# Kernel optimization log

Hardware: AMD Instinct MI355X
Metric: run time of the kernel (lower is better)

Reference implementation:

```python
import jax, jax.numpy as jnp
import numpy as np

HIDDEN = 1024
HEADS = 16
HEAD_DIM = HIDDEN // HEADS


def setup_inputs() -> dict:
    key = jax.random.key(0)
    ks = jax.random.split(key, 9)
    B, S = 2, 2048
    std = 1.0 / np.sqrt(HIDDEN)
    inp = {
        'hidden_states': jax.random.normal(ks[0], (B, S, HIDDEN), dtype=jnp.float32),
        'attention_mask': jnp.ones((B, S), dtype=jnp.int32),
        'wq': jax.random.normal(ks[1], (HIDDEN, HIDDEN), dtype=jnp.float32) * std,
        'bq': jnp.zeros((HIDDEN,), dtype=jnp.float32),
        'wk': jax.random.normal(ks[2], (HIDDEN, HIDDEN), dtype=jnp.float32) * std,
        'bk': jnp.zeros((HIDDEN,), dtype=jnp.float32),
        'wv': jax.random.normal(ks[3], (HIDDEN, HIDDEN), dtype=jnp.float32) * std,
        'bv': jnp.zeros((HIDDEN,), dtype=jnp.float32),
        'wo': jax.random.normal(ks[4], (HIDDEN, HIDDEN), dtype=jnp.float32) * std,
        'bo': jnp.zeros((HIDDEN,), dtype=jnp.float32),
    }
    return inp


def reference(hidden_states, attention_mask, wq, bq, wk, bk, wv, bv, wo, bo):
    B, S, H = hidden_states.shape
    def heads(x):  # [B,S,H] -> [B,nh,S,hd]
        return x.reshape(B, S, HEADS, HEAD_DIM).transpose(0, 2, 1, 3)
    q = heads(hidden_states @ wq + bq)
    k = heads(hidden_states @ wk + bk)
    v = heads(hidden_states @ wv + bv)
    scores = jnp.einsum('bhqd,bhkd->bhqk', q, k) / np.sqrt(HEAD_DIM).astype(np.float32)
    causal = jnp.tril(jnp.ones((S, S), dtype=bool))  # True = keep
    keep = causal[None, None] & (attention_mask[:, None, None, :] != 0)
    scores = jnp.where(keep, scores, -jnp.inf)
    probs = jax.nn.softmax(scores, axis=-1)
    out = jnp.einsum('bhqk,bhkd->bhqd', probs, v)  # [B,nh,S,hd]
    out = out.transpose(0, 2, 1, 3).reshape(B, S, H)
    return out @ wo + bo
```

## Files before the change

kernel.cpp:

```cpp
#include <hip/hip_runtime.h>

#define HID   1024
#define SLEN  2048
#define NHEAD 16
#define HDIM  64
#define SC2L  0.18033688f

typedef unsigned short u16;
typedef _Float16 f16;
using bf16x8 = __attribute__((ext_vector_type(8))) short;
using f16x4  = __attribute__((ext_vector_type(4))) f16;
using f32x4  = __attribute__((ext_vector_type(4))) float;

typedef __attribute__((address_space(1))) void gvoid;
typedef __attribute__((address_space(3))) void lvoid;

__device__ __forceinline__ u16 f2bf(float f) {
  union { float f; unsigned u; } v; v.f = f;
  unsigned u = v.u;
  return (u16)((u + 0x7fffu + ((u >> 16) & 1u)) >> 16);
}

__device__ __forceinline__ void async_ld16(const u16* g, u16* l) {
  __builtin_amdgcn_global_load_lds((gvoid*)g, (lvoid*)l, 16, 0, 0);
}

__global__ __launch_bounds__(256) void prep_kernel(const float* __restrict__ x,
                                                   const float* __restrict__ wq,
                                                   const float* __restrict__ wk,
                                                   const float* __restrict__ wv,
                                                   const float* __restrict__ wo,
                                                   u16* __restrict__ xb,
                                                   u16* __restrict__ wt) {
  const int tid = threadIdx.x;
  if (blockIdx.z == 4) {
    const int bid = blockIdx.y * 32 + blockIdx.x;
#pragma unroll
    for (int it = 0; it < 4; ++it) {
      const int i = bid * 1024 + it * 256 + tid;
      float4 v = ((const float4*)x)[i];
      ushort4 o;
      o.x = f2bf(v.x); o.y = f2bf(v.y); o.z = f2bf(v.z); o.w = f2bf(v.w);
      ((ushort4*)xb)[i] = o;
    }
    return;
  }
  const float* src = (blockIdx.z == 0) ? wq : (blockIdx.z == 1) ? wk
                   : (blockIdx.z == 2) ? wv : wo;
  u16* dst = wt + (size_t)blockIdx.z * (HID * HID);
  __shared__ float tile[32][33];
  const int n0 = blockIdx.x * 32, k0 = blockIdx.y * 32;
  const int xx = tid & 31, yy = tid >> 5;
  for (int i = yy; i < 32; i += 8)
    tile[i][xx] = src[(size_t)(k0 + i) * HID + n0 + xx];
  __syncthreads();
  for (int i = yy; i < 32; i += 8)
    dst[(size_t)(n0 + i) * HID + k0 + xx] = f2bf(tile[xx][i]);
}

__global__ __launch_bounds__(256) void gemm_qkv_kernel(const u16* __restrict__ A,
                                                       const u16* __restrict__ Bt,
                                                       const float* __restrict__ bq,
                                                       const float* __restrict__ bk,
                                                       const float* __restrict__ bv,
                                                       u16* __restrict__ Qb,
                                                       u16* __restrict__ Kb,
                                                       u16* __restrict__ VTf) {
  __shared__ u16 smem[16384];
  const int tid  = threadIdx.x;
  const int wave = tid >> 6, lane = tid & 63;
  const int quad = lane >> 4, l16 = lane & 15;
  const int raw = blockIdx.y * 24 + blockIdx.x;
  const int logi = (raw & 7) * 96 + (raw >> 3);
  const int bx = logi % 24, by = logi / 24;
  const int n0g = bx * 128;
  const int region = bx >> 3;
  const int colbase = (bx & 7) * 128;
  const int m0 = by * 128;
  const int wm = (wave & 1) * 64, wn = (wave >> 1) * 64;

  f32x4 acc[4][4] = {};
  const int srow = lane >> 2;
  const int scol = (lane & 3) * 8;

#define STAGE_G(kt, bi)                                                          \
  for (int c = wave; c < 8; c += 4) {                                            \
    async_ld16(A  + (size_t)(m0  + c * 16 + srow) * HID + (kt) + scol,           \
               &smem[(bi) * 8192 + c * 512]);                                    \
    async_ld16(Bt + (size_t)(n0g + c * 16 + srow) * HID + (kt) + scol,           \
               &smem[(bi) * 8192 + 4096 + c * 512]);                             \
  }

  STAGE_G(0, 0);
  for (int ks = 0; ks < 32; ++ks) {
    const int bi = ks & 1;
    if (ks < 31) {
      STAGE_G((ks + 1) * 32, bi ^ 1);
      asm volatile("s_waitcnt vmcnt(4)" ::: "memory");
    } else {
      asm volatile("s_waitcnt vmcnt(0)" ::: "memory");
    }
    __builtin_amdgcn_s_barrier();

    const u16* sA = smem + bi * 8192;
    const u16* sB = smem + bi * 8192 + 4096;
    bf16x8 af[4], bfr[4];
#pragma unroll
    for (int t = 0; t < 4; ++t) {
      af[t]  = *(const bf16x8*)&sA[(wm + t * 16 + l16) * 32 + quad * 8];
      bfr[t] = *(const bf16x8*)&sB[(wn + t * 16 + l16) * 32 + quad * 8];
    }
#pragma unroll
    for (int mt = 0; mt < 4; ++mt)
#pragma unroll
      for (int nt = 0; nt < 4; ++nt)
        acc[mt][nt] = __builtin_amdgcn_mfma_f32_16x16x32_bf16(af[mt], bfr[nt],
                                                              acc[mt][nt], 0, 0, 0);
    __builtin_amdgcn_s_barrier();
  }
#undef STAGE_G

  const float* bias = (region == 0) ? bq : (region == 1) ? bk : bv;
  float bvv[4];
#pragma unroll
  for (int nt = 0; nt < 4; ++nt) bvv[nt] = bias[colbase + wn + nt * 16 + l16];

  if (region == 2) {
    const int bb = m0 >> 11;
    const int m0loc = m0 & 2047;
    const int h0 = colbase >> 6;
    u16* T = smem;
#pragma unroll
    for (int h2 = 0; h2 < 2; ++h2) {
      __syncthreads();
      if ((wave >> 1) == h2) {
#pragma unroll
        for (int mt = 0; mt < 4; ++mt)
#pragma unroll
          for (int nt = 0; nt < 4; ++nt)
#pragma unroll
            for (int r = 0; r < 4; ++r) {
              const int sl = (wave & 1) * 64 + mt * 16 + quad * 4 + r;
              const int dl = nt * 16 + l16;
              union { f16 h; u16 u; } cv;
              cv.h = (f16)(acc[mt][nt][r] + bvv[nt]);
              T[dl * 128 + (((sl >> 3) ^ l16) * 8) + (sl & 7)] = cv.u;
            }
      }
      __syncthreads();
      const int d = tid >> 2, sg = (tid & 3) * 4;
      u16* slab0 = VTf + ((size_t)((bb * NHEAD + h0 + h2) * 128 + (m0loc >> 4))) * 1024;
#pragma unroll
      for (int cc = 0; cc < 4; ++cc) {
        const int cl = sg + cc;
        const int ph = cl ^ (d & 15);
        const int slot = (d * 2 + (cl & 1)) ^ ((d >> 2) & 1);
        *(bf16x8*)(slab0 + (size_t)(cl >> 1) * 1024 + slot * 8)
            = *(const bf16x8*)&T[d * 128 + ph * 8];
      }
    }
    return;
  }

  u16* C = (region == 0) ? Qb : Kb;
#pragma unroll
  for (int mt = 0; mt < 4; ++mt)
#pragma unroll
    for (int r = 0; r < 4; ++r) {
      const int row = m0 + wm + mt * 16 + quad * 4 + r;
#pragma unroll
      for (int nt = 0; nt < 4; ++nt) {
        const int col = colbase + wn + nt * 16 + l16;
        C[(size_t)row * HID + col] = f2bf(acc[mt][nt][r] + bvv[nt]);
      }
    }
}

__global__ __launch_bounds__(256) void gemm_o_kernel(const u16* __restrict__ A,
                                                     const u16* __restrict__ Bt,
                                                     const float* __restrict__ bias,
                                                     float* __restrict__ Cf) {
  __shared__ u16 smem[12288];
  const int tid  = threadIdx.x;
  const int wave = tid >> 6, lane = tid & 63;
  const int quad = lane >> 4, l16 = lane & 15;
  const int raw = blockIdx.y * 8 + blockIdx.x;
  const int logi = (raw & 7) * 64 + (raw >> 3);
  const int n0 = (logi & 7) * 128;
  const int m0 = (logi >> 3) * 64;
  const int wn = wave * 32;

  f32x4 acc[4][2] = {};
  const int srow = lane >> 2;
  const int scol = (lane & 3) * 8;

#define STAGE_O(kt, bi)                                                          \
  for (int c = wave; c < 12; c += 4) {                                           \
    if (c < 4) async_ld16(A + (size_t)(m0 + c * 16 + srow) * HID + (kt) + scol,  \
                          &smem[(bi) * 6144 + c * 512]);                         \
    else async_ld16(Bt + (size_t)(n0 + (c - 4) * 16 + srow) * HID + (kt) + scol, \
                    &smem[(bi) * 6144 + 2048 + (c - 4) * 512]);                  \
  }

  STAGE_O(0, 0);
  for (int ks = 0; ks < 32; ++ks) {
    const int bi = ks & 1;
    if (ks < 31) {
      STAGE_O((ks + 1) * 32, bi ^ 1);
      asm volatile("s_waitcnt vmcnt(3)" ::: "memory");
    } else {
      asm volatile("s_waitcnt vmcnt(0)" ::: "memory");
    }
    __builtin_amdgcn_s_barrier();

    const u16* sA = smem + bi * 6144;
    const u16* sB = smem + bi * 6144 + 2048;
    bf16x8 af[4], bfr[2];
#pragma unroll
    for (int t = 0; t < 4; ++t)
      af[t] = *(const bf16x8*)&sA[(t * 16 + l16) * 32 + quad * 8];
#pragma unroll
    for (int t = 0; t < 2; ++t)
      bfr[t] = *(const bf16x8*)&sB[(wn + t * 16 + l16) * 32 + quad * 8];
#pragma unroll
    for (int mt = 0; mt < 4; ++mt)
#pragma unroll
      for (int nt = 0; nt < 2; ++nt)
        acc[mt][nt] = __builtin_amdgcn_mfma_f32_16x16x32_bf16(af[mt], bfr[nt],
                                                              acc[mt][nt], 0, 0, 0);
    __builtin_amdgcn_s_barrier();
  }
#undef STAGE_O

  float bvv[2];
#pragma unroll
  for (int nt = 0; nt < 2; ++nt) bvv[nt] = bias[n0 + wn + nt * 16 + l16];
#pragma unroll
  for (int mt = 0; mt < 4; ++mt)
#pragma unroll
    for (int r = 0; r < 4; ++r) {
      const int row = m0 + mt * 16 + quad * 4 + r;
#pragma unroll
      for (int nt = 0; nt < 2; ++nt)
        Cf[(size_t)row * HID + n0 + wn + nt * 16 + l16] = acc[mt][nt][r] + bvv[nt];
    }
}

__global__ __launch_bounds__(256, 2) void flash_attn_kernel(const u16* __restrict__ Q,
                                                            const u16* __restrict__ K,
                                                            const u16* __restrict__ VT,
                                                            const int* __restrict__ mask,
                                                            u16* __restrict__ O) {
  const int xb = blockIdx.x, h = blockIdx.y, b = blockIdx.z;
  const int tid  = threadIdx.x;
  const int wave = tid >> 6, lane = tid & 63;
  const int quad = lane >> 4, l16 = lane & 15;

  __shared__ alignas(16) char smraw[35840];
  u16*   Ks  = (u16*)smraw;
  u16*   Vt  = (u16*)(smraw + 16384);
  float* Ob0 = (float*)smraw;
  float* Ob1 = (float*)(smraw + 16896);
  float* lb  = (float*)(smraw + 33792);

  const u16* Kh  = K  + (size_t)b * SLEN * HID + h * HDIM;
  const u16* Vth = VT + (size_t)(b * NHEAD + h) * (128 * 1024);

  const int srow8 = lane >> 3;
  const int gch   = (lane & 7) ^ srow8;
  const int rx    = l16 & 7;

  for (int phase = 0; phase < 2; ++phase) {
    const int qt = phase ? (31 - xb) : xb;
    const int q0 = qt * 64;

    bf16x8 qb[4][2];
#pragma unroll
    for (int nt = 0; nt < 4; ++nt) {
      const u16* qp = Q + (size_t)(b * SLEN + q0 + nt * 16 + l16) * HID + h * HDIM + quad * 8;
      qb[nt][0] = *(const bf16x8*)qp;
      qb[nt][1] = *(const bf16x8*)(qp + 32);
    }

    f32x4 oacc[4][4] = {};
    float l_part[4] = {0.f, 0.f, 0.f, 0.f};

    {
      const int r0 = wave * 16 + srow8;
      u16* kd = Ks + wave * 1024;
      async_ld16(Kh + (size_t)r0 * HID + gch * 8,       kd);
      async_ld16(Kh + (size_t)(r0 + 8) * HID + gch * 8, kd + 512);
      const u16* vs = Vth + (size_t)wave * 1024;
      u16* vd = Vt + wave * 1024;
      async_ld16(vs + lane * 8,        vd);
      async_ld16(vs + (64 + lane) * 8, vd + 512);
    }
    int4 mi = *(const int4*)(mask + b * SLEN + wave * 16 + quad * 4);

    for (int j = 0; j <= qt; ++j) {
      const int buf = j & 1;
      u16* KsB = Ks + buf * 4096;
      u16* VtB = Vt + buf * 4096;

      int4 mi_n = mi;
      if (j < qt) {
        const int nb = (buf ^ 1) * 4096;
        const int jn = j + 1;
        const int r0 = wave * 16 + srow8;
        u16* kd = Ks + nb + wave * 1024;
        async_ld16(Kh + (size_t)(jn * 64 + r0) * HID + gch * 8,     kd);
        async_ld16(Kh + (size_t)(jn * 64 + r0 + 8) * HID + gch * 8, kd + 512);
        const u16* vs = Vth + (size_t)(jn * 4 + wave) * 1024;
        u16* vd = Vt + nb + wave * 1024;
        async_ld16(vs + lane * 8,        vd);
        async_ld16(vs + (64 + lane) * 8, vd + 512);
        asm volatile("s_waitcnt vmcnt(4)" ::: "memory");
        mi_n = *(const int4*)(mask + b * SLEN + jn * 64 + wave * 16 + quad * 4);
      } else {
        asm volatile("s_waitcnt vmcnt(0)" ::: "memory");
      }

      float map[4];
      map[0] = mi.x ? 0.f : -1e30f;  map[1] = mi.y ? 0.f : -1e30f;
      map[2] = mi.z ? 0.f : -1e30f;  map[3] = mi.w ? 0.f : -1e30f;

      const u16* kp = KsB + (wave * 16 + l16) * 64;
      const int ph0 = quad ^ rx;
      const bf16x8 ka0 = *(const bf16x8*)(kp + ph0 * 8);
      const bf16x8 ka1 = *(const bf16x8*)(kp + (ph0 ^ 4) * 8);

      float p[4][4];
#pragma unroll
      for (int nt = 0; nt < 4; ++nt) {
        f32x4 z = {0.f, 0.f, 0.f, 0.f};
        z = __builtin_amdgcn_mfma_f32_16x16x32_bf16(ka0, qb[nt][0], z, 0, 0, 0);
        z = __builtin_amdgcn_mfma_f32_16x16x32_bf16(ka1, qb[nt][1], z, 0, 0, 0);
#pragma unroll
        for (int r = 0; r < 4; ++r)
          p[nt][r] = exp2f(fmaf(z[r], SC2L, map[r]));
      }
      if (j == qt) {
#pragma unroll
        for (int nt = 0; nt < 4; ++nt)
#pragma unroll
          for (int r = 0; r < 4; ++r)
            if (wave * 16 + quad * 4 + r > nt * 16 + l16) p[nt][r] = 0.f;
      }

      f16x4 pb[4];
#pragma unroll
      for (int nt = 0; nt < 4; ++nt) {
        l_part[nt] += (p[nt][0] + p[nt][1]) + (p[nt][2] + p[nt][3]);
        pb[nt][0] = (f16)p[nt][0]; pb[nt][1] = (f16)p[nt][1];
        pb[nt][2] = (f16)p[nt][2]; pb[nt][3] = (f16)p[nt][3];
      }

#pragma unroll
      for (int dt = 0; dt < 4; ++dt) {
        const int dd = dt * 16 + l16;
        const int slot = (dd * 2 + (quad >> 1)) ^ ((dd >> 2) & 1);
        const f16x4 va = *(const f16x4*)(VtB + wave * 1024 + slot * 8 + (quad & 1) * 4);
#pragma unroll
        for (int nt = 0; nt < 4; ++nt)
          oacc[dt][nt] = __builtin_amdgcn_mfma_f32_16x16x16f16(va, pb[nt], oacc[dt][nt], 0, 0, 0);
      }
      mi = mi_n;
    }

    __syncthreads();

#pragma unroll
    for (int nt = 0; nt < 4; ++nt) {
      l_part[nt] += __shfl_xor(l_part[nt], 16);
      l_part[nt] += __shfl_xor(l_part[nt], 32);
    }
    if (quad == 0)
#pragma unroll
      for (int nt = 0; nt < 4; ++nt) lb[wave * 64 + nt * 16 + l16] = l_part[nt];

    if ((wave & 1) == 0) {
      float* ob = (wave == 0) ? Ob0 : Ob1;
#pragma unroll
      for (int dt = 0; dt < 4; ++dt)
#pragma unroll
        for (int nt = 0; nt < 4; ++nt)
#pragma unroll
          for (int r = 0; r < 4; ++r)
            ob[(dt * 16 + quad * 4 + r) * 66 + nt * 16 + l16] = oacc[dt][nt][r];
    }
    __syncthreads();
    if (wave & 1) {
      float* ob = (wave == 1) ? Ob0 : Ob1;
#pragma unroll
      for (int dt = 0; dt < 4; ++dt)
#pragma unroll
        for (int nt = 0; nt < 4; ++nt)
#pragma unroll
          for (int r = 0; r < 4; ++r)
            ob[(dt * 16 + quad * 4 + r) * 66 + nt * 16 + l16] += oacc[dt][nt][r];
    }
    __syncthreads();

    {
      const int q  = tid >> 2;
      const int dc = tid & 3;
      const float l = lb[q] + lb[64 + q] + lb[128 + q] + lb[192 + q];
      const float inv = 1.f / l;
      u16 ob[16];
#pragma unroll
      for (int e = 0; e < 16; ++e) {
        const int d = dc * 16 + e;
        ob[e] = f2bf((Ob0[d * 66 + q] + Ob1[d * 66 + q]) * inv);
      }
      u16* op = O + (size_t)(b * SLEN + q0 + q) * HID + h * HDIM + dc * 16;
      *(bf16x8*)op       = *(bf16x8*)&ob[0];
      *(bf16x8*)(op + 8) = *(bf16x8*)&ob[8];
    }
    __syncthreads();
  }
}

extern "C" void kernel_launch(void* const* d_in, const int* in_sizes, int n_in,
                              void* d_out, int out_size, void* d_ws, size_t ws_size,
                              hipStream_t stream) {
  const float* x    = (const float*)d_in[0];
  const int*   mask = (const int*)d_in[1];
  const float* wq   = (const float*)d_in[2];
  const float* bq   = (const float*)d_in[3];
  const float* wk   = (const float*)d_in[4];
  const float* bk   = (const float*)d_in[5];
  const float* wv   = (const float*)d_in[6];
  const float* bv   = (const float*)d_in[7];
  const float* wo   = (const float*)d_in[8];
  const float* bo   = (const float*)d_in[9];
  float* out = (float*)d_out;

  char* ws = (char*)d_ws;
  u16* XBF = (u16*)(ws);
  u16* WT  = (u16*)(ws + (8u  << 20));
  u16* QBF = (u16*)(ws + (16u << 20));
  u16* KBF = (u16*)(ws + (24u << 20));
  u16* VTF = (u16*)(ws + (32u << 20));
  u16* ATT = (u16*)(ws);

  prep_kernel<<<dim3(32, 32, 5), 256, 0, stream>>>(x, wq, wk, wv, wo, XBF, WT);
  gemm_qkv_kernel<<<dim3(24, 32), 256, 0, stream>>>(XBF, WT, bq, bk, bv, QBF, KBF, VTF);
  flash_attn_kernel<<<dim3(16, NHEAD, 2), 256, 0, stream>>>(QBF, KBF, VTF, mask, ATT);
  gemm_o_kernel<<<dim3(8, 64), 256, 0, stream>>>(ATT, WT + (3u << 20), bo, out);
}
```

Before: 196.7 us.

## Use 8 waves and a 4-stage async load pipeline in QKV GEMM

The QKV projection GEMM now launches 512 threads per block. Each of the 8 waves computes a 64x32 sub-tile instead of a 64x64 one, and half the waves load A while the other half load B. The shared-memory ring goes from double to quad buffering, prefetching three k-steps ahead with adjusted vmcnt waits, to hide global load latency and raise wave occupancy. The cost is twice the LDS (64 KB per block), which may limit how many blocks fit per CU, and each wave issues fewer MFMAs per LDS fragment it reads.

```diff
diff --git a/kernel.cpp b/kernel.cpp
--- a/kernel.cpp
+++ b/kernel.cpp
@@ -58,7 +58,7 @@
     dst[(size_t)(n0 + i) * HID + k0 + xx] = f2bf(tile[xx][i]);
 }
 
-__global__ __launch_bounds__(256) void gemm_qkv_kernel(const u16* __restrict__ A,
+__global__ __launch_bounds__(512) void gemm_qkv_kernel(const u16* __restrict__ A,
                                                        const u16* __restrict__ Bt,
                                                        const float* __restrict__ bq,
                                                        const float* __restrict__ bk,
@@ -66,7 +66,7 @@
                                                        u16* __restrict__ Qb,
                                                        u16* __restrict__ Kb,
                                                        u16* __restrict__ VTf) {
-  __shared__ u16 smem[16384];
+  __shared__ u16 smem[32768];
   const int tid  = threadIdx.x;
   const int wave = tid >> 6, lane = tid & 63;
   const int quad = lane >> 4, l16 = lane & 15;
@@ -77,26 +77,42 @@
   const int region = bx >> 3;
   const int colbase = (bx & 7) * 128;
   const int m0 = by * 128;
-  const int wm = (wave & 1) * 64, wn = (wave >> 1) * 64;
-
-  f32x4 acc[4][4] = {};
+  const int wm = (wave & 1) * 64;
+  const int wn = (wave >> 1) * 32;
+
+  f32x4 acc[4][2] = {};
   const int srow = lane >> 2;
   const int scol = (lane & 3) * 8;
 
 #define STAGE_G(kt, bi)                                                          \
-  for (int c = wave; c < 8; c += 4) {                                            \
-    async_ld16(A  + (size_t)(m0  + c * 16 + srow) * HID + (kt) + scol,           \
-               &smem[(bi) * 8192 + c * 512]);                                    \
-    async_ld16(Bt + (size_t)(n0g + c * 16 + srow) * HID + (kt) + scol,           \
-               &smem[(bi) * 8192 + 4096 + c * 512]);                             \
+  {                                                                              \
+    u16* dstb = smem + (bi) * 8192;                                              \
+    const int c0 = 2 * wave, c1 = 2 * wave + 1;                                  \
+    if (wave < 4) {                                                              \
+      async_ld16(A + (size_t)(m0 + c0 * 16 + srow) * HID + (kt) + scol,          \
+                 &dstb[c0 * 512]);                                               \
+      async_ld16(A + (size_t)(m0 + c1 * 16 + srow) * HID + (kt) + scol,          \
+                 &dstb[c1 * 512]);                                               \
+    } else {                                                                     \
+      async_ld16(Bt + (size_t)(n0g + (c0 - 8) * 16 + srow) * HID + (kt) + scol,  \
+                 &dstb[4096 + (c0 - 8) * 512]);                                  \
+      async_ld16(Bt + (size_t)(n0g + (c1 - 8) * 16 + srow) * HID + (kt) + scol,  \
+                 &dstb[4096 + (c1 - 8) * 512]);                                  \
+    }                                                                            \
   }
 
   STAGE_G(0, 0);
+  STAGE_G(32, 1);
+  STAGE_G(64, 2);
   for (int ks = 0; ks < 32; ++ks) {
-    const int bi = ks & 1;
-    if (ks < 31) {
-      STAGE_G((ks + 1) * 32, bi ^ 1);
+    const int bi = ks & 3;
+    if (ks <= 28) {
+      STAGE_G((ks + 3) * 32, (ks + 3) & 3);
+      asm volatile("s_waitcnt vmcnt(6)" ::: "memory");
+    } else if (ks == 29) {
       asm volatile("s_waitcnt vmcnt(4)" ::: "memory");
+    } else if (ks == 30) {
+      asm volatile("s_waitcnt vmcnt(2)" ::: "memory");
     } else {
       asm volatile("s_waitcnt vmcnt(0)" ::: "memory");
     }
@@ -104,16 +120,17 @@
 
     const u16* sA = smem + bi * 8192;
     const u16* sB = smem + bi * 8192 + 4096;
-    bf16x8 af[4], bfr[4];
-#pragma unroll
-    for (int t = 0; t < 4; ++t) {
+    bf16x8 af[4], bfr[2];
+#pragma unroll
+    for (int t = 0; t < 4; ++t)
       af[t]  = *(const bf16x8*)&sA[(wm + t * 16 + l16) * 32 + quad * 8];
+#pragma unroll
+    for (int t = 0; t < 2; ++t)
       bfr[t] = *(const bf16x8*)&sB[(wn + t * 16 + l16) * 32 + quad * 8];
-    }
 #pragma unroll
     for (int mt = 0; mt < 4; ++mt)
 #pragma unroll
-      for (int nt = 0; nt < 4; ++nt)
+      for (int nt = 0; nt < 2; ++nt)
         acc[mt][nt] = __builtin_amdgcn_mfma_f32_16x16x32_bf16(af[mt], bfr[nt],
                                                               acc[mt][nt], 0, 0, 0);
     __builtin_amdgcn_s_barrier();
@@ -121,9 +138,9 @@
 #undef STAGE_G
 
   const float* bias = (region == 0) ? bq : (region == 1) ? bk : bv;
-  float bvv[4];
-#pragma unroll
-  for (int nt = 0; nt < 4; ++nt) bvv[nt] = bias[colbase + wn + nt * 16 + l16];
+  float bvv[2];
+#pragma unroll
+  for (int nt = 0; nt < 2; ++nt) bvv[nt] = bias[colbase + wn + nt * 16 + l16];
 
   if (region == 2) {
     const int bb = m0 >> 11;
@@ -133,25 +150,25 @@
 #pragma unroll
     for (int h2 = 0; h2 < 2; ++h2) {
       __syncthreads();
-      if ((wave >> 1) == h2) {
+      if ((wave >> 2) == h2) {
 #pragma unroll
         for (int mt = 0; mt < 4; ++mt)
 #pragma unroll
-          for (int nt = 0; nt < 4; ++nt)
+          for (int nt = 0; nt < 2; ++nt)
 #pragma unroll
             for (int r = 0; r < 4; ++r) {
-              const int sl = (wave & 1) * 64 + mt * 16 + quad * 4 + r;
-              const int dl = nt * 16 + l16;
+              const int sl = wm + mt * 16 + quad * 4 + r;
+              const int dl = (wn & 32) + nt * 16 + l16;
               union { f16 h; u16 u; } cv;
               cv.h = (f16)(acc[mt][nt][r] + bvv[nt]);
               T[dl * 128 + (((sl >> 3) ^ l16) * 8) + (sl & 7)] = cv.u;
             }
       }
       __syncthreads();
-      const int d = tid >> 2, sg = (tid & 3) * 4;
+      const int d = tid >> 3, sg = (tid & 7) * 2;
       u16* slab0 = VTf + ((size_t)((bb * NHEAD + h0 + h2) * 128 + (m0loc >> 4))) * 1024;
 #pragma unroll
-      for (int cc = 0; cc < 4; ++cc) {
+      for (int cc = 0; cc < 2; ++cc) {
         const int cl = sg + cc;
         const int ph = cl ^ (d & 15);
         const int slot = (d * 2 + (cl & 1)) ^ ((d >> 2) & 1);
@@ -169,7 +186,7 @@
     for (int r = 0; r < 4; ++r) {
       const int row = m0 + wm + mt * 16 + quad * 4 + r;
 #pragma unroll
-      for (int nt = 0; nt < 4; ++nt) {
+      for (int nt = 0; nt < 2; ++nt) {
         const int col = colbase + wn + nt * 16 + l16;
         C[(size_t)row * HID + col] = f2bf(acc[mt][nt][r] + bvv[nt]);
       }
@@ -444,7 +461,7 @@
   u16* ATT = (u16*)(ws);
 
   prep_kernel<<<dim3(32, 32, 5), 256, 0, stream>>>(x, wq, wk, wv, wo, XBF, WT);
-  gemm_qkv_kernel<<<dim3(24, 32), 256, 0, stream>>>(XBF, WT, bq, bk, bv, QBF, KBF, VTF);
+  gemm_qkv_kernel<<<dim3(24, 32), 512, 0, stream>>>(XBF, WT, bq, bk, bv, QBF, KBF, VTF);
   flash_attn_kernel<<<dim3(16, NHEAD, 2), 256, 0, stream>>>(QBF, KBF, VTF, mask, ATT);
   gemm_o_kernel<<<dim3(8, 64), 256, 0, stream>>>(ATT, WT + (3u << 20), bo, out);
 }
```

Measured after the change: 198.4 us. No clear change (+0.8%).
